# Kernel optimization log

Hardware: AMD Instinct MI355X
Metric: run time of the kernel (lower is better)

Reference implementation:

```python
import jax, jax.numpy as jnp
import numpy as np

N = 100000
E = 1600000
D_IN = 128
D_HID = 128
D_OUT = 64


def setup_inputs() -> dict:
    key = jax.random.key(0)
    ks = jax.random.split(key, 12)
    x = jax.random.normal(ks[0], (N, D_IN), dtype=jnp.float32)
    src = jax.random.randint(ks[1], (E,), 0, N, dtype=jnp.int32)
    dst = jax.random.randint(ks[2], (E,), 0, N, dtype=jnp.int32)
    def lin(k, din, dout):
        s = 1.0 / np.sqrt(din)
        return jax.random.uniform(k, (din, dout), jnp.float32, -s, s)
    return {
        "x": x, "src": src, "dst": dst,
        "Ws0": lin(ks[3], D_IN, D_HID), "Wn0": lin(ks[4], D_IN, D_HID), "b0": jnp.zeros((D_HID,), jnp.float32),
        "Ws1": lin(ks[5], D_HID, D_HID), "Wn1": lin(ks[6], D_HID, D_HID), "b1": jnp.zeros((D_HID,), jnp.float32),
        "Ws2": lin(ks[7], D_HID, D_OUT), "Wn2": lin(ks[8], D_HID, D_OUT), "b2": jnp.zeros((D_OUT,), jnp.float32),
    }


def _sage_conv(h, src, dst, Ws, Wn, b):
    # mean aggregation of neighbor (src) features onto dst nodes
    deg = jax.ops.segment_sum(jnp.ones((src.shape[0],), h.dtype), dst, num_segments=N)
    agg = jax.ops.segment_sum(h[src], dst, num_segments=N)  # [N, d_in]
    mean = agg / jnp.maximum(deg, 1.0)[:, None]
    return h @ Ws + mean @ Wn + b


def reference(x, src, dst, Ws0, Wn0, b0, Ws1, Wn1, b1, Ws2, Wn2, b2):
    h = _sage_conv(x, src, dst, Ws0, Wn0, b0)
    h = jax.nn.relu(h)  # dropout is identity in eval mode
    h = _sage_conv(h, src, dst, Ws1, Wn1, b1)
    h = jax.nn.relu(h)
    h = _sage_conv(h, src, dst, Ws2, Wn2, b2)
    return h
```

## Files before the change

kernel.cpp:

```cpp
#include <hip/hip_runtime.h>

#define NN 100000
#define NE 1600000
#define DF 128
#define TS 136
#define NCB 391
#define NWA 256
#define SZA 6250
#define NH (NCB * NWA)
#define CAPB 6144

typedef unsigned int uint32;
typedef unsigned short u16;
typedef _Float16 f16;
typedef f16 f16x8 __attribute__((ext_vector_type(8)));
typedef f16 f16x2 __attribute__((ext_vector_type(2)));
typedef float f32x4 __attribute__((ext_vector_type(4)));

__device__ __forceinline__ float2 up2(uint32 u) {
    union { uint32 u; f16x2 h; } v; v.u = u;
    return make_float2((float)v.h.x, (float)v.h.y);
}
__device__ __forceinline__ uint32 pk2(float a, float b) {
    union { f16x2 h; uint32 u; } v;
    v.h.x = (f16)a; v.h.y = (f16)b;
    return v.u;
}
__device__ __forceinline__ u16 f2h(float a) {
    union { f16 h; u16 u; } v; v.h = (f16)a; return v.u;
}
__device__ __forceinline__ float h2f(u16 a) {
    union { u16 u; f16 h; } v; v.u = a; return (float)v.h;
}


__global__ __launch_bounds__(256) void histA(const int* __restrict__ dst,
                                             int* __restrict__ H) {
    __shared__ int lh[NCB];
    int w = blockIdx.x, t = threadIdx.x;
    for (int i = t; i < NCB; i += 256) lh[i] = 0;
    __syncthreads();
    int e0 = w * SZA, e1 = min(e0 + SZA, NE);
    for (int e = e0 + t; e < e1; e += 256) atomicAdd(&lh[dst[e] >> 8], 1);
    __syncthreads();
    for (int i = t; i < NCB; i += 256) H[i * NWA + w] = lh[i];
}

__global__ __launch_bounds__(256) void sumCB(const int* __restrict__ H,
                                             int* __restrict__ CBT) {
    __shared__ int sm[256];
    int cb = blockIdx.x, t = threadIdx.x;
    sm[t] = H[cb * NWA + t];
    __syncthreads();
    for (int off = 128; off > 0; off >>= 1) {
        if (t < off) sm[t] += sm[t + off];
        __syncthreads();
    }
    if (t == 0) CBT[cb] = sm[0];
}

__global__ __launch_bounds__(512) void scanCB(const int* __restrict__ CBT,
                                              int* __restrict__ CBO,
                                              int* __restrict__ O,
                                              int* __restrict__ rowptr) {
    __shared__ int sm[512];
    int t = threadIdx.x;
    int v = (t < NCB) ? CBT[t] : 0;
    sm[t] = v;
    __syncthreads();
    for (int off = 1; off < 512; off <<= 1) {
        int x = (t >= off) ? sm[t - off] : 0;
        __syncthreads();
        sm[t] += x;
        __syncthreads();
    }
    if (t < NCB) CBO[t] = sm[t] - v;
    if (t == NCB - 1) {
        O[NH] = sm[t];
        rowptr[NN] = sm[t];
    }
}

__global__ __launch_bounds__(256) void scanW(const int* __restrict__ H,
                                             const int* __restrict__ CBO,
                                             int* __restrict__ O) {
    __shared__ int sm[256];
    int cb = blockIdx.x, t = threadIdx.x;
    int v = H[cb * NWA + t];
    sm[t] = v;
    __syncthreads();
    for (int off = 1; off < 256; off <<= 1) {
        int x = (t >= off) ? sm[t - off] : 0;
        __syncthreads();
        sm[t] += x;
        __syncthreads();
    }
    O[cb * NWA + t] = CBO[cb] + sm[t] - v;
}

__global__ __launch_bounds__(1024) void passA(const int* __restrict__ src,
                                              const int* __restrict__ dst,
                                              const int* __restrict__ O,
                                              uint32* __restrict__ ebuf) {
    __shared__ int cur[NCB];
    int w = blockIdx.x, t = threadIdx.x;
    for (int i = t; i < NCB; i += 1024) cur[i] = O[i * NWA + w];
    __syncthreads();
    int e0 = w * SZA, e1 = min(e0 + SZA, NE);
    for (int e = e0 + t; e < e1; e += 1024) {
        int d = dst[e];
        int cb = d >> 8;
        int p = atomicAdd(&cur[cb], 1);
        ebuf[p] = ((uint32)src[e] << 8) | (uint32)(d & 255);
    }
}

__global__ __launch_bounds__(256) void passB(const uint32* __restrict__ ebuf,
                                             const int* __restrict__ O,
                                             int* __restrict__ rowptr,
                                             int* __restrict__ col) {
    __shared__ int hist[256], start[256], cur[256];
    __shared__ int seg[CAPB];
    int cb = blockIdx.x, t = threadIdx.x;
    int base = O[cb * NWA], end = O[(cb + 1) * NWA];
    int m = end - base;
    hist[t] = 0;
    __syncthreads();
    for (int i = t; i < m; i += 256) atomicAdd(&hist[ebuf[base + i] & 255], 1);
    __syncthreads();
    int v = hist[t];
    cur[t] = v;
    __syncthreads();
    for (int off = 1; off < 256; off <<= 1) {
        int x = (t >= off) ? cur[t - off] : 0;
        __syncthreads();
        cur[t] += x;
        __syncthreads();
    }
    start[t] = cur[t] - v;
    __syncthreads();
    int node = cb * 256 + t;
    if (node < NN) rowptr[node] = base + start[t];
    cur[t] = start[t];
    __syncthreads();
    if (m <= CAPB) {
        for (int i = t; i < m; i += 256) {
            uint32 u = ebuf[base + i];
            int p = atomicAdd(&cur[u & 255], 1);
            seg[p] = (int)(u >> 8);
        }
        __syncthreads();
        for (int i = t; i < m; i += 256) col[base + i] = seg[i];
    } else {
        for (int i = t; i < m; i += 256) {
            uint32 u = ebuf[base + i];
            int p = atomicAdd(&cur[u & 255], 1);
            col[base + p] = (int)(u >> 8);
        }
    }
}

__global__ void prep_all(const float* __restrict__ Ws0, const float* __restrict__ Wn0,
                         const float* __restrict__ Ws1, const float* __restrict__ Wn1,
                         const float* __restrict__ Ws2, const float* __restrict__ Wn2,
                         u16* __restrict__ WB) {
    int t = blockIdx.x * 256 + threadIdx.x;
    if (t < 65536) {
        int m = t >> 14;
        int local = t & 16383;
        int k = local >> 7, n = local & 127;
        const float* W = (m == 0) ? Ws0 : (m == 1) ? Wn0 : (m == 2) ? Ws1 : Wn1;
        WB[m * 16384 + n * 128 + k] = f2h(W[k * 128 + n]);
    } else {
        int local = t - 65536;
        int half = local >> 13;
        int idx = local & 8191;
        int k = idx >> 6, n = idx & 63;
        const float* W = half ? Wn2 : Ws2;
        WB[4 * 16384 + (n + half * 64) * 128 + k] = f2h(W[k * 64 + n]);
    }
}

__global__ void cvt_f16(const float* __restrict__ x, uint2* __restrict__ xh) {
    int t = blockIdx.x * 256 + threadIdx.x;
    if (t < NN * DF / 4) {
        float4 v = ((const float4*)x)[t];
        uint2 o;
        o.x = pk2(v.x, v.y);
        o.y = pk2(v.z, v.w);
        xh[t] = o;
    }
}

__global__ __launch_bounds__(256) void gather_f16(const u16* __restrict__ hb,
                                                  const int* __restrict__ rowptr,
                                                  const int* __restrict__ col,
                                                  u16* __restrict__ mean) {
    int bid = blockIdx.x;
    int panel = bid & 1;
    int node = (bid >> 1) * 32 + (threadIdx.x >> 3);
    int g = threadIdx.x & 7;
    const u16* hp = hb + panel * 64 + g * 8;
    int s = rowptr[node], e = rowptr[node + 1];
    float acc[8];
#pragma unroll
    for (int i = 0; i < 8; ++i) acc[i] = 0.f;
    int j = s;
    for (; j + 7 < e; j += 8) {
        int n0 = col[j],     n1 = col[j + 1], n2 = col[j + 2], n3 = col[j + 3];
        int n4 = col[j + 4], n5 = col[j + 5], n6 = col[j + 6], n7 = col[j + 7];
        f16x8 v0 = *(const f16x8*)(hp + (size_t)n0 * DF);
        f16x8 v1 = *(const f16x8*)(hp + (size_t)n1 * DF);
        f16x8 v2 = *(const f16x8*)(hp + (size_t)n2 * DF);
        f16x8 v3 = *(const f16x8*)(hp + (size_t)n3 * DF);
        f16x8 v4 = *(const f16x8*)(hp + (size_t)n4 * DF);
        f16x8 v5 = *(const f16x8*)(hp + (size_t)n5 * DF);
        f16x8 v6 = *(const f16x8*)(hp + (size_t)n6 * DF);
        f16x8 v7 = *(const f16x8*)(hp + (size_t)n7 * DF);
        f16x8 sA = (v0 + v1) + (v2 + v3);
        f16x8 sB = (v4 + v5) + (v6 + v7);
#pragma unroll
        for (int i = 0; i < 8; ++i) acc[i] += (float)sA[i] + (float)sB[i];
    }
    for (; j + 3 < e; j += 4) {
        int n0 = col[j], n1 = col[j + 1], n2 = col[j + 2], n3 = col[j + 3];
        f16x8 v0 = *(const f16x8*)(hp + (size_t)n0 * DF);
        f16x8 v1 = *(const f16x8*)(hp + (size_t)n1 * DF);
        f16x8 v2 = *(const f16x8*)(hp + (size_t)n2 * DF);
        f16x8 v3 = *(const f16x8*)(hp + (size_t)n3 * DF);
        f16x8 sv = (v0 + v1) + (v2 + v3);
#pragma unroll
        for (int i = 0; i < 8; ++i) acc[i] += (float)sv[i];
    }
    for (; j < e; ++j) {
        f16x8 v = *(const f16x8*)(hp + (size_t)col[j] * DF);
#pragma unroll
        for (int i = 0; i < 8; ++i) acc[i] += (float)v[i];
    }
    float invd = 1.f / fmaxf((float)(e - s), 1.f);
    union { f16x8 h; uint4 u; } o;
#pragma unroll
    for (int i = 0; i < 8; ++i) o.h[i] = (f16)(acc[i] * invd);
    *(uint4*)(mean + (size_t)node * DF + panel * 64 + g * 8) = o.u;
}

__global__ __launch_bounds__(256) void gather_add_f16(const u16* __restrict__ gb,
                                                      const int* __restrict__ rowptr,
                                                      const int* __restrict__ col,
                                                      float* __restrict__ out) {
    int node = blockIdx.x * 32 + (threadIdx.x >> 3);
    int g = threadIdx.x & 7;
    int s = rowptr[node], e = rowptr[node + 1];
    float acc[8];
#pragma unroll
    for (int i = 0; i < 8; ++i) acc[i] = 0.f;
    int j = s;
    for (; j + 7 < e; j += 8) {
        int n0 = col[j],     n1 = col[j + 1], n2 = col[j + 2], n3 = col[j + 3];
        int n4 = col[j + 4], n5 = col[j + 5], n6 = col[j + 6], n7 = col[j + 7];
        f16x8 v0 = *(const f16x8*)(gb + (size_t)n0 * 64 + g * 8);
        f16x8 v1 = *(const f16x8*)(gb + (size_t)n1 * 64 + g * 8);
        f16x8 v2 = *(const f16x8*)(gb + (size_t)n2 * 64 + g * 8);
        f16x8 v3 = *(const f16x8*)(gb + (size_t)n3 * 64 + g * 8);
        f16x8 v4 = *(const f16x8*)(gb + (size_t)n4 * 64 + g * 8);
        f16x8 v5 = *(const f16x8*)(gb + (size_t)n5 * 64 + g * 8);
        f16x8 v6 = *(const f16x8*)(gb + (size_t)n6 * 64 + g * 8);
        f16x8 v7 = *(const f16x8*)(gb + (size_t)n7 * 64 + g * 8);
        f16x8 sA = (v0 + v1) + (v2 + v3);
        f16x8 sB = (v4 + v5) + (v6 + v7);
#pragma unroll
        for (int i = 0; i < 8; ++i) acc[i] += (float)sA[i] + (float)sB[i];
    }
    for (; j + 3 < e; j += 4) {
        int n0 = col[j], n1 = col[j + 1], n2 = col[j + 2], n3 = col[j + 3];
        f16x8 v0 = *(const f16x8*)(gb + (size_t)n0 * 64 + g * 8);
        f16x8 v1 = *(const f16x8*)(gb + (size_t)n1 * 64 + g * 8);
        f16x8 v2 = *(const f16x8*)(gb + (size_t)n2 * 64 + g * 8);
        f16x8 v3 = *(const f16x8*)(gb + (size_t)n3 * 64 + g * 8);
        f16x8 sv = (v0 + v1) + (v2 + v3);
#pragma unroll
        for (int i = 0; i < 8; ++i) acc[i] += (float)sv[i];
    }
    for (; j < e; ++j) {
        f16x8 v = *(const f16x8*)(gb + (size_t)col[j] * 64 + g * 8);
#pragma unroll
        for (int i = 0; i < 8; ++i) acc[i] += (float)v[i];
    }
    float invd = 1.f / fmaxf((float)(e - s), 1.f);
    float4* op = (float4*)(out + (size_t)node * 64 + g * 8);
    float4 a = op[0], b = op[1];
    a.x += acc[0] * invd; a.y += acc[1] * invd;
    a.z += acc[2] * invd; a.w += acc[3] * invd;
    b.x += acc[4] * invd; b.y += acc[5] * invd;
    b.z += acc[6] * invd; b.w += acc[7] * invd;
    op[0] = a; op[1] = b;
}

__device__ __forceinline__ void stage_a(u16* sm, const u16* g, int row0, int tid) {
#pragma unroll
    for (int i = 0; i < 8; ++i) {
        int idx = i * 256 + tid;
        int r = idx >> 4, c = (idx & 15) * 8;
        uint4 v = make_uint4(0, 0, 0, 0);
        int gr = row0 + r;
        if (gr < NN) v = *(const uint4*)(g + (size_t)gr * DF + c);
        *(uint4*)(sm + r * TS + c) = v;
    }
}

__device__ __forceinline__ void stage_w(u16* sm, const u16* wt, int nbase, int tid) {
#pragma unroll
    for (int i = 0; i < 4; ++i) {
        int idx = i * 256 + tid;
        int r = idx >> 4, c = (idx & 15) * 8;
        *(uint4*)(sm + r * TS + c) = *(const uint4*)(wt + (size_t)(nbase + r) * 128 + c);
    }
}

__device__ __forceinline__ f16x8 frag(const u16* sm, int row, int lane, int kc) {
    return *(const f16x8*)(sm + (row + (lane & 15)) * TS + kc * 32 + (lane >> 4) * 8);
}

__device__ __forceinline__ void mfma4(const u16* As, const u16* Bs, int wrow, int lane,
                                      f32x4 acc[2][8], int ab) {
    f16x8 a[2][4];
#pragma unroll
    for (int rt = 0; rt < 2; ++rt)
#pragma unroll
        for (int kc = 0; kc < 4; ++kc) a[rt][kc] = frag(As, wrow + rt * 16, lane, kc);
#pragma unroll
    for (int n = 0; n < 4; ++n) {
#pragma unroll
        for (int kc = 0; kc < 4; ++kc) {
            f16x8 b = frag(Bs, n * 16, lane, kc);
            acc[0][ab + n] = __builtin_amdgcn_mfma_f32_16x16x32_f16(a[0][kc], b, acc[0][ab + n], 0, 0, 0);
            acc[1][ab + n] = __builtin_amdgcn_mfma_f32_16x16x32_f16(a[1][kc], b, acc[1][ab + n], 0, 0, 0);
        }
    }
}

#define SW(WT, NB) { __syncthreads(); stage_w(Bs, WT, NB, tid); __syncthreads(); }

__global__ __launch_bounds__(256) void gemm_sage_f16(
    const u16* H, const u16* M,
    const u16* __restrict__ Ws, const u16* __restrict__ Wn,
    const float* __restrict__ bias, u16* OutH) {
    __shared__ u16 As[128 * TS];
    __shared__ u16 Bs[64 * TS];
    const int tid = threadIdx.x;
    const int lane = tid & 63;
    const int wrow = (tid >> 6) * 32;
    const int row0 = blockIdx.x * 128;

    f32x4 acc[2][8];
#pragma unroll
    for (int rt = 0; rt < 2; ++rt)
#pragma unroll
        for (int n = 0; n < 8; ++n) acc[rt][n] = {0.f, 0.f, 0.f, 0.f};

    stage_a(As, H, row0, tid);
    stage_w(Bs, Ws, 0, tid);
    __syncthreads();
    mfma4(As, Bs, wrow, lane, acc, 0);
    SW(Ws, 64); mfma4(As, Bs, wrow, lane, acc, 4);
    __syncthreads();
    stage_a(As, M, row0, tid);
    stage_w(Bs, Wn, 0, tid);
    __syncthreads();
    mfma4(As, Bs, wrow, lane, acc, 0);
    SW(Wn, 64); mfma4(As, Bs, wrow, lane, acc, 4);

    const int cit = lane & 15;
    const int rq = (lane >> 4) * 4;
#pragma unroll
    for (int rt = 0; rt < 2; ++rt)
#pragma unroll
        for (int n = 0; n < 8; ++n) {
            float bv = bias[n * 16 + cit];
            f32x4 v = acc[rt][n];
#pragma unroll
            for (int r = 0; r < 4; ++r) {
                int gr = row0 + wrow + rt * 16 + rq + r;
                if (gr < NN) {
                    float o = fmaxf(v[r] + bv, 0.f);
                    OutH[(size_t)gr * DF + n * 16 + cit] = f2h(o);
                }
            }
        }
}

__global__ __launch_bounds__(256) void gemm_l2_f16(
    const u16* __restrict__ H, const u16* __restrict__ W2,
    const float* __restrict__ b2, float* __restrict__ out, u16* __restrict__ g2) {
    __shared__ u16 As[128 * TS];
    __shared__ u16 Bs[64 * TS];
    const int tid = threadIdx.x;
    const int lane = tid & 63;
    const int wrow = (tid >> 6) * 32;
    const int row0 = blockIdx.x * 128;

    f32x4 acc[2][8];
#pragma unroll
    for (int rt = 0; rt < 2; ++rt)
#pragma unroll
        for (int n = 0; n < 8; ++n) acc[rt][n] = {0.f, 0.f, 0.f, 0.f};

    stage_a(As, H, row0, tid);
    stage_w(Bs, W2, 0, tid);
    __syncthreads();
    mfma4(As, Bs, wrow, lane, acc, 0);
    SW(W2, 64); mfma4(As, Bs, wrow, lane, acc, 4);

    const int cit = lane & 15;
    const int rq = (lane >> 4) * 4;
#pragma unroll
    for (int rt = 0; rt < 2; ++rt)
#pragma unroll
        for (int n = 0; n < 8; ++n) {
            f32x4 v = acc[rt][n];
            float bv = (n < 4) ? b2[n * 16 + cit] : 0.f;
#pragma unroll
            for (int r = 0; r < 4; ++r) {
                int gr = row0 + wrow + rt * 16 + rq + r;
                if (gr < NN) {
                    if (n < 4) out[(size_t)gr * 64 + n * 16 + cit] = v[r] + bv;
                    else g2[(size_t)gr * 64 + (n - 4) * 16 + cit] = f2h(v[r]);
                }
            }
        }
}

extern "C" void kernel_launch(void* const* d_in, const int* in_sizes, int n_in,
                              void* d_out, int out_size, void* d_ws, size_t ws_size,
                              hipStream_t stream) {
    const float* x   = (const float*)d_in[0];
    const int*   src = (const int*)d_in[1];
    const int*   dst = (const int*)d_in[2];
    const float* Ws0 = (const float*)d_in[3];
    const float* Wn0 = (const float*)d_in[4];
    const float* b0  = (const float*)d_in[5];
    const float* Ws1 = (const float*)d_in[6];
    const float* Wn1 = (const float*)d_in[7];
    const float* b1  = (const float*)d_in[8];
    const float* Ws2 = (const float*)d_in[9];
    const float* Wn2 = (const float*)d_in[10];
    const float* b2  = (const float*)d_in[11];
    float* out = (float*)d_out;

    int* H       = (int*)d_ws;
    int* O       = H + NH;
    int* CBT     = O + 100352;
    int* CBO     = CBT + 512;
    int* rowptr  = CBO + 512;
    int* col     = rowptr + 100352;
    uint32* ebuf = (uint32*)(col + NE);
    u16* WB      = (u16*)(ebuf + NE);
    u16* W0s = WB, *W0n = WB + 16384, *W1s = WB + 2 * 16384, *W1n = WB + 3 * 16384;
    u16* W2  = WB + 4 * 16384;
    u16* P1 = WB + 5 * 16384;
    u16* P3 = P1 + (size_t)NN * DF;

    const int gB = (NN + 127) / 128;

    histA<<<NWA, 256, 0, stream>>>(dst, H);
    sumCB<<<NCB, 256, 0, stream>>>(H, CBT);
    scanCB<<<1, 512, 0, stream>>>(CBT, CBO, O, rowptr);
    scanW<<<NCB, 256, 0, stream>>>(H, CBO, O);
    passA<<<NWA, 1024, 0, stream>>>(src, dst, O, ebuf);
    passB<<<NCB, 256, 0, stream>>>(ebuf, O, rowptr, col);

    prep_all<<<320, 256, 0, stream>>>(Ws0, Wn0, Ws1, Wn1, Ws2, Wn2, WB);

    cvt_f16<<<NN * DF / 4 / 256, 256, 0, stream>>>(x, (uint2*)P1);

    gather_f16<<<(NN / 32) * 2, 256, 0, stream>>>(P1, rowptr, col, P3);
    gemm_sage_f16<<<gB, 256, 0, stream>>>(P1, P3, W0s, W0n, b0, P1);

    gather_f16<<<(NN / 32) * 2, 256, 0, stream>>>(P1, rowptr, col, P3);
    gemm_sage_f16<<<gB, 256, 0, stream>>>(P1, P3, W1s, W1n, b1, P1);

    gemm_l2_f16<<<gB, 256, 0, stream>>>(P1, W2, b2, out, P3);
    gather_add_f16<<<NN / 32, 256, 0, stream>>>(P3, rowptr, col, out);
}
```

Measured before the change: 379.0 us.

## Fuse neighbor-mean gather into SAGE GEMM and merge small prep kernels

Each SAGE layer's mean aggregation now runs inside the GEMM kernel: every block gathers and averages neighbor rows for its 128 nodes straight into shared memory, then runs the MFMA tiles. This drops the separate gather kernel and the round trip of the mean matrix through global memory. The two scan kernels are merged into one, and the weight prep and input conversion share a single launch. In exchange, only 782 blocks do the latency-bound gather with less parallelism and no overlap with the MFMA work. Outputs now ping-pong between buffers instead of being written in place.

Measured after the change: 428.6 us. 13.1% more time.

```diff
diff --git a/kernel.cpp b/kernel.cpp
--- a/kernel.cpp
+++ b/kernel.cpp
@@ -17,10 +17,6 @@
 typedef f16 f16x2 __attribute__((ext_vector_type(2)));
 typedef float f32x4 __attribute__((ext_vector_type(4)));
 
-__device__ __forceinline__ float2 up2(uint32 u) {
-    union { uint32 u; f16x2 h; } v; v.u = u;
-    return make_float2((float)v.h.x, (float)v.h.y);
-}
 __device__ __forceinline__ uint32 pk2(float a, float b) {
     union { f16x2 h; uint32 u; } v;
     v.h.x = (f16)a; v.h.y = (f16)b;
@@ -28,9 +24,6 @@
 }
 __device__ __forceinline__ u16 f2h(float a) {
     union { f16 h; u16 u; } v; v.h = (f16)a; return v.u;
-}
-__device__ __forceinline__ float h2f(u16 a) {
-    union { u16 u; f16 h; } v; v.u = a; return (float)v.h;
 }
 
 
@@ -59,12 +52,13 @@
     if (t == 0) CBT[cb] = sm[0];
 }
 
-__global__ __launch_bounds__(512) void scanCB(const int* __restrict__ CBT,
-                                              int* __restrict__ CBO,
-                                              int* __restrict__ O,
-                                              int* __restrict__ rowptr) {
+__global__ __launch_bounds__(512) void scanCBW(const int* __restrict__ CBT,
+                                               const int* __restrict__ H,
+                                               int* __restrict__ O,
+                                               int* __restrict__ rowptr) {
     __shared__ int sm[512];
-    int t = threadIdx.x;
+    __shared__ int sh[256];
+    int cb = blockIdx.x, t = threadIdx.x;
     int v = (t < NCB) ? CBT[t] : 0;
     sm[t] = v;
     __syncthreads();
@@ -74,28 +68,21 @@
         sm[t] += x;
         __syncthreads();
     }
-    if (t < NCB) CBO[t] = sm[t] - v;
-    if (t == NCB - 1) {
+    if (cb == 0 && t == NCB - 1) {
         O[NH] = sm[t];
         rowptr[NN] = sm[t];
     }
-}
-
-__global__ __launch_bounds__(256) void scanW(const int* __restrict__ H,
-                                             const int* __restrict__ CBO,
-                                             int* __restrict__ O) {
-    __shared__ int sm[256];
-    int cb = blockIdx.x, t = threadIdx.x;
-    int v = H[cb * NWA + t];
-    sm[t] = v;
+    int cbo = sm[cb] - CBT[cb];
+    int hv = (t < 256) ? H[cb * NWA + t] : 0;
+    if (t < 256) sh[t] = hv;
     __syncthreads();
     for (int off = 1; off < 256; off <<= 1) {
-        int x = (t >= off) ? sm[t - off] : 0;
-        __syncthreads();
-        sm[t] += x;
-        __syncthreads();
-    }
-    O[cb * NWA + t] = CBO[cb] + sm[t] - v;
+        int x = (t >= off && t < 256) ? sh[t - off] : 0;
+        __syncthreads();
+        if (t < 256) sh[t] += x;
+        __syncthreads();
+    }
+    if (t < 256) O[cb * NWA + t] = cbo + sh[t] - hv;
 }
 
 __global__ __launch_bounds__(1024) void passA(const int* __restrict__ src,
@@ -160,88 +147,38 @@
     }
 }
 
-__global__ void prep_all(const float* __restrict__ Ws0, const float* __restrict__ Wn0,
+__global__ void prep_cvt(const float* __restrict__ Ws0, const float* __restrict__ Wn0,
                          const float* __restrict__ Ws1, const float* __restrict__ Wn1,
                          const float* __restrict__ Ws2, const float* __restrict__ Wn2,
-                         u16* __restrict__ WB) {
-    int t = blockIdx.x * 256 + threadIdx.x;
-    if (t < 65536) {
-        int m = t >> 14;
-        int local = t & 16383;
-        int k = local >> 7, n = local & 127;
-        const float* W = (m == 0) ? Ws0 : (m == 1) ? Wn0 : (m == 2) ? Ws1 : Wn1;
-        WB[m * 16384 + n * 128 + k] = f2h(W[k * 128 + n]);
+                         u16* __restrict__ WB,
+                         const float* __restrict__ x, uint2* __restrict__ xh) {
+    int b = blockIdx.x;
+    if (b < 320) {
+        int t = b * 256 + threadIdx.x;
+        if (t < 65536) {
+            int m = t >> 14;
+            int local = t & 16383;
+            int k = local >> 7, n = local & 127;
+            const float* W = (m == 0) ? Ws0 : (m == 1) ? Wn0 : (m == 2) ? Ws1 : Wn1;
+            WB[m * 16384 + n * 128 + k] = f2h(W[k * 128 + n]);
+        } else {
+            int local = t - 65536;
+            int half = local >> 13;
+            int idx = local & 8191;
+            int k = idx >> 6, n = idx & 63;
+            const float* W = half ? Wn2 : Ws2;
+            WB[4 * 16384 + (n + half * 64) * 128 + k] = f2h(W[k * 64 + n]);
+        }
     } else {
-        int local = t - 65536;
-        int half = local >> 13;
-        int idx = local & 8191;
-        int k = idx >> 6, n = idx & 63;
-        const float* W = half ? Wn2 : Ws2;
-        WB[4 * 16384 + (n + half * 64) * 128 + k] = f2h(W[k * 64 + n]);
-    }
-}
-
-__global__ void cvt_f16(const float* __restrict__ x, uint2* __restrict__ xh) {
-    int t = blockIdx.x * 256 + threadIdx.x;
-    if (t < NN * DF / 4) {
-        float4 v = ((const float4*)x)[t];
-        uint2 o;
-        o.x = pk2(v.x, v.y);
-        o.y = pk2(v.z, v.w);
-        xh[t] = o;
-    }
-}
-
-__global__ __launch_bounds__(256) void gather_f16(const u16* __restrict__ hb,
-                                                  const int* __restrict__ rowptr,
-                                                  const int* __restrict__ col,
-                                                  u16* __restrict__ mean) {
-    int bid = blockIdx.x;
-    int panel = bid & 1;
-    int node = (bid >> 1) * 32 + (threadIdx.x >> 3);
-    int g = threadIdx.x & 7;
-    const u16* hp = hb + panel * 64 + g * 8;
-    int s = rowptr[node], e = rowptr[node + 1];
-    float acc[8];
-#pragma unroll
-    for (int i = 0; i < 8; ++i) acc[i] = 0.f;
-    int j = s;
-    for (; j + 7 < e; j += 8) {
-        int n0 = col[j],     n1 = col[j + 1], n2 = col[j + 2], n3 = col[j + 3];
-        int n4 = col[j + 4], n5 = col[j + 5], n6 = col[j + 6], n7 = col[j + 7];
-        f16x8 v0 = *(const f16x8*)(hp + (size_t)n0 * DF);
-        f16x8 v1 = *(const f16x8*)(hp + (size_t)n1 * DF);
-        f16x8 v2 = *(const f16x8*)(hp + (size_t)n2 * DF);
-        f16x8 v3 = *(const f16x8*)(hp + (size_t)n3 * DF);
-        f16x8 v4 = *(const f16x8*)(hp + (size_t)n4 * DF);
-        f16x8 v5 = *(const f16x8*)(hp + (size_t)n5 * DF);
-        f16x8 v6 = *(const f16x8*)(hp + (size_t)n6 * DF);
-        f16x8 v7 = *(const f16x8*)(hp + (size_t)n7 * DF);
-        f16x8 sA = (v0 + v1) + (v2 + v3);
-        f16x8 sB = (v4 + v5) + (v6 + v7);
-#pragma unroll
-        for (int i = 0; i < 8; ++i) acc[i] += (float)sA[i] + (float)sB[i];
-    }
-    for (; j + 3 < e; j += 4) {
-        int n0 = col[j], n1 = col[j + 1], n2 = col[j + 2], n3 = col[j + 3];
-        f16x8 v0 = *(const f16x8*)(hp + (size_t)n0 * DF);
-        f16x8 v1 = *(const f16x8*)(hp + (size_t)n1 * DF);
-        f16x8 v2 = *(const f16x8*)(hp + (size_t)n2 * DF);
-        f16x8 v3 = *(const f16x8*)(hp + (size_t)n3 * DF);
-        f16x8 sv = (v0 + v1) + (v2 + v3);
-#pragma unroll
-        for (int i = 0; i < 8; ++i) acc[i] += (float)sv[i];
-    }
-    for (; j < e; ++j) {
-        f16x8 v = *(const f16x8*)(hp + (size_t)col[j] * DF);
-#pragma unroll
-        for (int i = 0; i < 8; ++i) acc[i] += (float)v[i];
-    }
-    float invd = 1.f / fmaxf((float)(e - s), 1.f);
-    union { f16x8 h; uint4 u; } o;
-#pragma unroll
-    for (int i = 0; i < 8; ++i) o.h[i] = (f16)(acc[i] * invd);
-    *(uint4*)(mean + (size_t)node * DF + panel * 64 + g * 8) = o.u;
+        int t = (b - 320) * 256 + threadIdx.x;
+        if (t < NN * DF / 4) {
+            float4 v = ((const float4*)x)[t];
+            uint2 o;
+            o.x = pk2(v.x, v.y);
+            o.y = pk2(v.z, v.w);
+            xh[t] = o;
+        }
+    }
 }
 
 __global__ __launch_bounds__(256) void gather_add_f16(const u16* __restrict__ gb,
@@ -341,10 +278,71 @@
 
 #define SW(WT, NB) { __syncthreads(); stage_w(Bs, WT, NB, tid); __syncthreads(); }
 
-__global__ __launch_bounds__(256) void gemm_sage_f16(
-    const u16* H, const u16* M,
+__device__ __forceinline__ void gather_As(u16* As, const u16* __restrict__ hb,
+                                          const int* __restrict__ rowptr,
+                                          const int* __restrict__ col,
+                                          int row0, int tid) {
+    int g = tid & 15;
+    int rb = tid >> 4;
+    const u16* hp = hb + g * 8;
+#pragma unroll 1
+    for (int p = 0; p < 8; ++p) {
+        int r = p * 16 + rb;
+        int gr = row0 + r;
+        union { f16x8 h; uint4 u; } o;
+        if (gr < NN) {
+            int s = rowptr[gr], e = rowptr[gr + 1];
+            float acc[8];
+#pragma unroll
+            for (int i = 0; i < 8; ++i) acc[i] = 0.f;
+            int j = s;
+            for (; j + 7 < e; j += 8) {
+                int n0 = col[j],     n1 = col[j + 1], n2 = col[j + 2], n3 = col[j + 3];
+                int n4 = col[j + 4], n5 = col[j + 5], n6 = col[j + 6], n7 = col[j + 7];
+                f16x8 v0 = *(const f16x8*)(hp + (size_t)n0 * DF);
+                f16x8 v1 = *(const f16x8*)(hp + (size_t)n1 * DF);
+                f16x8 v2 = *(const f16x8*)(hp + (size_t)n2 * DF);
+                f16x8 v3 = *(const f16x8*)(hp + (size_t)n3 * DF);
+                f16x8 v4 = *(const f16x8*)(hp + (size_t)n4 * DF);
+                f16x8 v5 = *(const f16x8*)(hp + (size_t)n5 * DF);
+                f16x8 v6 = *(const f16x8*)(hp + (size_t)n6 * DF);
+                f16x8 v7 = *(const f16x8*)(hp + (size_t)n7 * DF);
+                f16x8 sA = (v0 + v1) + (v2 + v3);
+                f16x8 sB = (v4 + v5) + (v6 + v7);
+#pragma unroll
+                for (int i = 0; i < 8; ++i) acc[i] += (float)sA[i] + (float)sB[i];
+            }
+            for (; j + 3 < e; j += 4) {
+                int n0 = col[j], n1 = col[j + 1], n2 = col[j + 2], n3 = col[j + 3];
+                f16x8 v0 = *(const f16x8*)(hp + (size_t)n0 * DF);
+                f16x8 v1 = *(const f16x8*)(hp + (size_t)n1 * DF);
+                f16x8 v2 = *(const f16x8*)(hp + (size_t)n2 * DF);
+                f16x8 v3 = *(const f16x8*)(hp + (size_t)n3 * DF);
+                f16x8 sv = (v0 + v1) + (v2 + v3);
+#pragma unroll
+                for (int i = 0; i < 8; ++i) acc[i] += (float)sv[i];
+            }
+            for (; j < e; ++j) {
+                f16x8 v = *(const f16x8*)(hp + (size_t)col[j] * DF);
+#pragma unroll
+                for (int i = 0; i < 8; ++i) acc[i] += (float)v[i];
+            }
+            float invd = 1.f / fmaxf((float)(e - s), 1.f);
+#pragma unroll
+            for (int i = 0; i < 8; ++i) o.h[i] = (f16)(acc[i] * invd);
+        } else {
+            o.u = make_uint4(0, 0, 0, 0);
+        }
+        *(uint4*)(As + r * TS + g * 8) = o.u;
+    }
+}
+
+__global__ __launch_bounds__(256) void fused_sage_f16(
+    const u16* __restrict__ Hin,
     const u16* __restrict__ Ws, const u16* __restrict__ Wn,
-    const float* __restrict__ bias, u16* OutH) {
+    const float* __restrict__ bias,
+    const int* __restrict__ rowptr, const int* __restrict__ col,
+    u16* __restrict__ OutH) {
     __shared__ u16 As[128 * TS];
     __shared__ u16 Bs[64 * TS];
     const int tid = threadIdx.x;
@@ -352,23 +350,24 @@
     const int wrow = (tid >> 6) * 32;
     const int row0 = blockIdx.x * 128;
 
+    stage_w(Bs, Wn, 0, tid);
+    gather_As(As, Hin, rowptr, col, row0, tid);
+    __syncthreads();
+
     f32x4 acc[2][8];
 #pragma unroll
     for (int rt = 0; rt < 2; ++rt)
 #pragma unroll
         for (int n = 0; n < 8; ++n) acc[rt][n] = {0.f, 0.f, 0.f, 0.f};
 
-    stage_a(As, H, row0, tid);
+    mfma4(As, Bs, wrow, lane, acc, 0);
+    SW(Wn, 64); mfma4(As, Bs, wrow, lane, acc, 4);
+    __syncthreads();
+    stage_a(As, Hin, row0, tid);
     stage_w(Bs, Ws, 0, tid);
     __syncthreads();
     mfma4(As, Bs, wrow, lane, acc, 0);
     SW(Ws, 64); mfma4(As, Bs, wrow, lane, acc, 4);
-    __syncthreads();
-    stage_a(As, M, row0, tid);
-    stage_w(Bs, Wn, 0, tid);
-    __syncthreads();
-    mfma4(As, Bs, wrow, lane, acc, 0);
-    SW(Wn, 64); mfma4(As, Bs, wrow, lane, acc, 4);
 
     const int cit = lane & 15;
     const int rq = (lane >> 4) * 4;
@@ -464,20 +463,16 @@
 
     histA<<<NWA, 256, 0, stream>>>(dst, H);
     sumCB<<<NCB, 256, 0, stream>>>(H, CBT);
-    scanCB<<<1, 512, 0, stream>>>(CBT, CBO, O, rowptr);
-    scanW<<<NCB, 256, 0, stream>>>(H, CBO, O);
+    scanCBW<<<NCB, 512, 0, stream>>>(CBT, H, O, rowptr);
     passA<<<NWA, 1024, 0, stream>>>(src, dst, O, ebuf);
     passB<<<NCB, 256, 0, stream>>>(ebuf, O, rowptr, col);
 
-    prep_all<<<320, 256, 0, stream>>>(Ws0, Wn0, Ws1, Wn1, Ws2, Wn2, WB);
-
-    cvt_f16<<<NN * DF / 4 / 256, 256, 0, stream>>>(x, (uint2*)P1);
-
-    gather_f16<<<(NN / 32) * 2, 256, 0, stream>>>(P1, rowptr, col, P3);
-    gemm_sage_f16<<<gB, 256, 0, stream>>>(P1, P3, W0s, W0n, b0, P1);
-
-    gather_f16<<<(NN / 32) * 2, 256, 0, stream>>>(P1, rowptr, col, P3);
-    gemm_sage_f16<<<gB, 256, 0, stream>>>(P1, P3, W1s, W1n, b1, P1);
+    prep_cvt<<<320 + NN * DF / 4 / 256, 256, 0, stream>>>(
+        Ws0, Wn0, Ws1, Wn1, Ws2, Wn2, WB, x, (uint2*)P1);
+
+    fused_sage_f16<<<gB, 256, 0, stream>>>(P1, W0s, W0n, b0, rowptr, col, P3);
+
+    fused_sage_f16<<<gB, 256, 0, stream>>>(P3, W1s, W1n, b1, rowptr, col, P1);
 
     gemm_l2_f16<<<gB, 256, 0, stream>>>(P1, W2, b2, out, P3);
     gather_add_f16<<<NN / 32, 256, 0, stream>>>(P3, rowptr, col, out);
```
